# Optimization experiments

Hardware: AMD Instinct MI355X
Metric: run time of the kernel (lower is better)

## Reference

```python
import jax, jax.numpy as jnp
import numpy as np

DELTA_V = 0.5
DELTA_D = 1.5
KSEG = 17  # segment ids 0..16 (0 = background)
EPS = 1e-12


def setup_inputs() -> dict:
    key = jax.random.key(0)
    k1, k2, k3 = jax.random.split(key, 3)
    B, C, H, W = 8, 8, 512, 512
    embeddings = jax.random.normal(k1, (B, C, H, W), dtype=jnp.float32)
    instance_labels = jax.random.randint(k2, (B, H, W), 0, KSEG, dtype=jnp.int32)
    mask = jax.random.randint(k3, (B, H, W), 0, 2, dtype=jnp.int32)
    return {"embeddings": embeddings, "instance_labels": instance_labels, "mask": mask}


def _discriminative_loss(embeddings, inst):
    # embeddings: (B, C, H, W); inst: (B, H, W) int, 0 = ignore/background
    B, C, H, W = embeddings.shape
    N = H * W
    ids = inst.reshape(B, N)
    # global segment ids so one segment_sum handles all batches
    gids = (ids + jnp.arange(B, dtype=ids.dtype)[:, None] * KSEG).reshape(-1)  # (B*N,)
    e = embeddings.reshape(B, C, N).transpose(0, 2, 1).reshape(B * N, C)       # (B*N, C)

    counts = jax.ops.segment_sum(jnp.ones((B * N,), embeddings.dtype), gids, num_segments=B * KSEG)
    sums = jax.ops.segment_sum(e, gids, num_segments=B * KSEG)                 # (B*KSEG, C)
    means = sums / jnp.maximum(counts, 1.0)[:, None]

    # ---- pull: per-pixel hinged distance to its instance mean ----
    diff = e - means[gids]                                                      # (B*N, C)
    d = jnp.sqrt(jnp.maximum(jnp.sum(diff * diff, axis=-1), EPS))               # (B*N,)
    pen = jnp.maximum(d - DELTA_V, 0.0) ** 2
    pen_mean = jax.ops.segment_sum(pen, gids, num_segments=B * KSEG) / jnp.maximum(counts, 1.0)

    counts_bk = counts.reshape(B, KSEG)
    pen_mean_bk = pen_mean.reshape(B, KSEG)
    present = (counts_bk > 0) & (jnp.arange(KSEG)[None, :] != 0)                # (B, KSEG) bool
    presentf = present.astype(embeddings.dtype)
    K = presentf.sum(axis=-1)                                                   # (B,) instances per image
    pull_b = (pen_mean_bk * presentf).sum(axis=-1) / jnp.maximum(K, 1.0)

    # ---- push: hinged pairwise mean distances ----
    mu = means.reshape(B, KSEG, C)
    dm = mu[:, :, None, :] - mu[:, None, :, :]                                  # (B, K, K, C)
    dist = jnp.sqrt(jnp.maximum(jnp.sum(dm * dm, axis=-1), EPS))
    hinge = jnp.maximum(2.0 * DELTA_D - dist, 0.0) ** 2
    iu = jnp.triu(jnp.ones((KSEG, KSEG), bool), k=1)                            # i < j
    pair_mask = (present[:, :, None] & present[:, None, :] & iu[None]).astype(embeddings.dtype)
    n_pairs = pair_mask.sum(axis=(-1, -2))
    push_b = (hinge * pair_mask).sum(axis=(-1, -2)) / jnp.maximum(n_pairs, 1.0)

    validf = (K > 0).astype(embeddings.dtype)
    nvalid = jnp.maximum(validf.sum(), 1.0)
    loss_pull = (pull_b * validf).sum() / nvalid
    loss_push = (push_b * validf).sum() / nvalid
    return loss_pull, loss_push


def reference(embeddings, instance_labels, mask):
    inst = instance_labels * mask  # zero out non-TCL pixels
    return _discriminative_loss(embeddings, inst)
```

## Files before the change

kernel.cpp:

```cpp
#include <hip/hip_runtime.h>

#define BATCH 8
#define CCH 8
#define HW 262144
#define SEGS 16


__global__ __launch_bounds__(256) void accum_kernel(
    const float* __restrict__ emb, const int* __restrict__ lab,
    const int* __restrict__ msk, float* __restrict__ ws)
{
    const int b = blockIdx.y;
    const int wave = threadIdx.x >> 6;
    __shared__ float lsum[4][SEGS][CCH];
    __shared__ float lcnt[4][SEGS];
    for (int i = threadIdx.x; i < 4 * SEGS * CCH; i += 256) (&lsum[0][0][0])[i] = 0.f;
    for (int i = threadIdx.x; i < 4 * SEGS; i += 256) (&lcnt[0][0])[i] = 0.f;
    __syncthreads();

    const float* eb = emb + (size_t)b * CCH * HW;
    const int4* lb = (const int4*)(lab + (size_t)b * HW);
    const int4* mb = (const int4*)(msk + (size_t)b * HW);

    const int ng = HW / 4;
    for (int g = blockIdx.x * 256 + threadIdx.x; g < ng; g += gridDim.x * 256) {
        int4 l4 = lb[g];
        int4 m4 = mb[g];
        int id[4];
        id[0] = m4.x ? l4.x : 0;
        id[1] = m4.y ? l4.y : 0;
        id[2] = m4.z ? l4.z : 0;
        id[3] = m4.w ? l4.w : 0;
#pragma unroll
        for (int j = 0; j < 4; ++j)
            if (id[j]) atomicAdd(&lcnt[wave][id[j] - 1], 1.0f);
#pragma unroll
        for (int c = 0; c < CCH; ++c) {
            float4 e4 = ((const float4*)(eb + (size_t)c * HW))[g];
            float ev[4] = {e4.x, e4.y, e4.z, e4.w};
#pragma unroll
            for (int j = 0; j < 4; ++j)
                if (id[j]) atomicAdd(&lsum[wave][id[j] - 1][c], ev[j]);
        }
    }
    __syncthreads();
    for (int i = threadIdx.x; i < SEGS * CCH; i += 256) {
        float v = (&lsum[0][0][0])[i] + (&lsum[1][0][0])[i]
                + (&lsum[2][0][0])[i] + (&lsum[3][0][0])[i];
        if (v != 0.f) atomicAdd(&ws[128 + b * SEGS * CCH + i], v);
    }
    for (int i = threadIdx.x; i < SEGS; i += 256) {
        float v = lcnt[0][i] + lcnt[1][i] + lcnt[2][i] + lcnt[3][i];
        if (v != 0.f) atomicAdd(&ws[b * SEGS + i], v);
    }
}

__global__ __launch_bounds__(256) void pull_kernel(
    const float* __restrict__ emb, const int* __restrict__ lab,
    const int* __restrict__ msk, float* __restrict__ ws)
{
    const int b = blockIdx.y;
    const int wave = threadIdx.x >> 6;
    __shared__ float mt[CCH][SEGS];
    __shared__ float lpen[4][SEGS];
    for (int i = threadIdx.x; i < 4 * SEGS; i += 256) (&lpen[0][0])[i] = 0.f;
    if (threadIdx.x < SEGS * CCH) {
        int s = threadIdx.x & (SEGS - 1);
        int c = threadIdx.x >> 4;
        float cnt = ws[b * SEGS + s];
        mt[c][s] = ws[128 + (b * SEGS + s) * CCH + c] / fmaxf(cnt, 1.0f);
    }
    __syncthreads();

    const float* eb = emb + (size_t)b * CCH * HW;
    const int4* lb = (const int4*)(lab + (size_t)b * HW);
    const int4* mb = (const int4*)(msk + (size_t)b * HW);

    const int ng = HW / 4;
    for (int g = blockIdx.x * 256 + threadIdx.x; g < ng; g += gridDim.x * 256) {
        int4 l4 = lb[g];
        int4 m4 = mb[g];
        int id[4];
        id[0] = m4.x ? l4.x : 0;
        id[1] = m4.y ? l4.y : 0;
        id[2] = m4.z ? l4.z : 0;
        id[3] = m4.w ? l4.w : 0;
        int ix[4];
#pragma unroll
        for (int j = 0; j < 4; ++j) ix[j] = id[j] ? id[j] - 1 : 0;
        float ss[4] = {0.f, 0.f, 0.f, 0.f};
#pragma unroll
        for (int c = 0; c < CCH; ++c) {
            float4 e4 = ((const float4*)(eb + (size_t)c * HW))[g];
            float ev[4] = {e4.x, e4.y, e4.z, e4.w};
#pragma unroll
            for (int j = 0; j < 4; ++j) {
                float d = ev[j] - mt[c][ix[j]];
                ss[j] += d * d;
            }
        }
#pragma unroll
        for (int j = 0; j < 4; ++j) {
            if (id[j]) {
                float d = sqrtf(fmaxf(ss[j], 1e-12f));
                float h = fmaxf(d - 0.5f, 0.f);
                atomicAdd(&lpen[wave][ix[j]], h * h);
            }
        }
    }
    __syncthreads();
    for (int i = threadIdx.x; i < SEGS; i += 256) {
        float v = lpen[0][i] + lpen[1][i] + lpen[2][i] + lpen[3][i];
        if (v != 0.f) atomicAdd(&ws[1152 + b * SEGS + i], v);
    }
}

__global__ __launch_bounds__(256) void finalize_kernel(
    const float* __restrict__ ws, float* __restrict__ out)
{
    __shared__ float cnt[BATCH][SEGS];
    __shared__ float mu[BATCH][SEGS][CCH];
    __shared__ float pen[BATCH][SEGS];
    __shared__ float res[BATCH][3];

    for (int i = threadIdx.x; i < BATCH * SEGS; i += 256) {
        (&cnt[0][0])[i] = ws[i];
        (&pen[0][0])[i] = ws[1152 + i];
    }
    for (int i = threadIdx.x; i < BATCH * SEGS * CCH; i += 256) {
        float c = ws[i / CCH];
        (&mu[0][0][0])[i] = ws[128 + i] / fmaxf(c, 1.0f);
    }
    __syncthreads();

    const int b = threadIdx.x >> 5;
    const int l = threadIdx.x & 31;

    float pullv = 0.f, Kf = 0.f;
    if (l < SEGS && cnt[b][l] > 0.f) {
        Kf = 1.f;
        pullv = pen[b][l] / cnt[b][l];
    }
    float hs = 0.f, np = 0.f;
    for (int p = l; p < 256; p += 32) {
        int i = p >> 4, j = p & 15;
        if (i < j && cnt[b][i] > 0.f && cnt[b][j] > 0.f) {
            float ssq = 0.f;
#pragma unroll
            for (int c = 0; c < CCH; ++c) {
                float d = mu[b][i][c] - mu[b][j][c];
                ssq += d * d;
            }
            float dist = sqrtf(fmaxf(ssq, 1e-12f));
            float h = fmaxf(3.0f - dist, 0.f);
            hs += h * h;
            np += 1.f;
        }
    }
#pragma unroll
    for (int m = 16; m >= 1; m >>= 1) {
        pullv += __shfl_xor(pullv, m);
        Kf    += __shfl_xor(Kf, m);
        hs    += __shfl_xor(hs, m);
        np    += __shfl_xor(np, m);
    }
    if (l == 0) {
        res[b][0] = (Kf > 0.f) ? pullv / Kf : 0.f;
        res[b][1] = (np > 0.f) ? hs / np : 0.f;
        res[b][2] = (Kf > 0.f) ? 1.f : 0.f;
    }
    __syncthreads();
    if (threadIdx.x == 0) {
        float sp = 0.f, sh = 0.f, nv = 0.f;
        for (int bb = 0; bb < BATCH; ++bb) {
            sp += res[bb][0] * res[bb][2];
            sh += res[bb][1] * res[bb][2];
            nv += res[bb][2];
        }
        nv = fmaxf(nv, 1.f);
        out[0] = sp / nv;
        out[1] = sh / nv;
    }
}

extern "C" void kernel_launch(void* const* d_in, const int* in_sizes, int n_in,
                              void* d_out, int out_size, void* d_ws, size_t ws_size,
                              hipStream_t stream)
{
    const float* emb = (const float*)d_in[0];
    const int* lab = (const int*)d_in[1];
    const int* msk = (const int*)d_in[2];
    float* out = (float*)d_out;
    float* ws = (float*)d_ws;

    hipMemsetAsync(d_ws, 0, 1280 * sizeof(float), stream);
    dim3 grid(128, BATCH);
    accum_kernel<<<grid, 256, 0, stream>>>(emb, lab, msk, ws);
    pull_kernel<<<grid, 256, 0, stream>>>(emb, lab, msk, ws);
    finalize_kernel<<<1, 256, 0, stream>>>(ws, out);
}
```

Measured before the change: 156.7 us.

## Replicate shared histograms per 16 threads and assign one pixel group per thread

Shared-memory histograms for sums, counts and penalties are replicated 16 times per block (one copy per 16 threads) with padded strides, instead of one copy per wave. This is meant to reduce LDS atomic contention when many lanes hit the same segment. The grid doubles so each thread processes exactly one 4-pixel group, removing the grid-stride loop. The cost is a larger final reduction over 16 copies and twice as many global atomics per batch.

Result: slower. 170.8 us (+9.0%).

```diff
diff --git a/kernel.cpp b/kernel.cpp
--- a/kernel.cpp
+++ b/kernel.cpp
@@ -4,6 +4,9 @@
 #define CCH 8
 #define HW 262144
 #define SEGS 16
+#define NREP 16
+#define RSTRIDE 132
+#define CSTRIDE 17
 
 
 __global__ __launch_bounds__(256) void accum_kernel(
@@ -11,47 +14,51 @@
     const int* __restrict__ msk, float* __restrict__ ws)
 {
     const int b = blockIdx.y;
-    const int wave = threadIdx.x >> 6;
-    __shared__ float lsum[4][SEGS][CCH];
-    __shared__ float lcnt[4][SEGS];
-    for (int i = threadIdx.x; i < 4 * SEGS * CCH; i += 256) (&lsum[0][0][0])[i] = 0.f;
-    for (int i = threadIdx.x; i < 4 * SEGS; i += 256) (&lcnt[0][0])[i] = 0.f;
+    const int rep = threadIdx.x >> 4;
+    __shared__ float lsum[NREP * RSTRIDE];
+    __shared__ float lcnt[NREP * CSTRIDE];
+    for (int i = threadIdx.x; i < NREP * RSTRIDE; i += 256) lsum[i] = 0.f;
+    for (int i = threadIdx.x; i < NREP * CSTRIDE; i += 256) lcnt[i] = 0.f;
     __syncthreads();
 
     const float* eb = emb + (size_t)b * CCH * HW;
-    const int4* lb = (const int4*)(lab + (size_t)b * HW);
-    const int4* mb = (const int4*)(msk + (size_t)b * HW);
-
-    const int ng = HW / 4;
-    for (int g = blockIdx.x * 256 + threadIdx.x; g < ng; g += gridDim.x * 256) {
-        int4 l4 = lb[g];
-        int4 m4 = mb[g];
-        int id[4];
-        id[0] = m4.x ? l4.x : 0;
-        id[1] = m4.y ? l4.y : 0;
-        id[2] = m4.z ? l4.z : 0;
-        id[3] = m4.w ? l4.w : 0;
+    const int g = blockIdx.x * 256 + threadIdx.x;
+    int4 l4 = ((const int4*)(lab + (size_t)b * HW))[g];
+    int4 m4 = ((const int4*)(msk + (size_t)b * HW))[g];
+    int id[4];
+    id[0] = m4.x ? l4.x : 0;
+    id[1] = m4.y ? l4.y : 0;
+    id[2] = m4.z ? l4.z : 0;
+    id[3] = m4.w ? l4.w : 0;
+
+    float* ls = lsum + rep * RSTRIDE;
+    float* lc = lcnt + rep * CSTRIDE;
+#pragma unroll
+    for (int j = 0; j < 4; ++j)
+        if (id[j]) atomicAdd(&lc[id[j] - 1], 1.0f);
+#pragma unroll
+    for (int c = 0; c < CCH; ++c) {
+        float4 e4 = ((const float4*)(eb + (size_t)c * HW))[g];
+        float ev[4] = {e4.x, e4.y, e4.z, e4.w};
 #pragma unroll
         for (int j = 0; j < 4; ++j)
-            if (id[j]) atomicAdd(&lcnt[wave][id[j] - 1], 1.0f);
-#pragma unroll
-        for (int c = 0; c < CCH; ++c) {
-            float4 e4 = ((const float4*)(eb + (size_t)c * HW))[g];
-            float ev[4] = {e4.x, e4.y, e4.z, e4.w};
-#pragma unroll
-            for (int j = 0; j < 4; ++j)
-                if (id[j]) atomicAdd(&lsum[wave][id[j] - 1][c], ev[j]);
-        }
-    }
-    __syncthreads();
-    for (int i = threadIdx.x; i < SEGS * CCH; i += 256) {
-        float v = (&lsum[0][0][0])[i] + (&lsum[1][0][0])[i]
-                + (&lsum[2][0][0])[i] + (&lsum[3][0][0])[i];
-        if (v != 0.f) atomicAdd(&ws[128 + b * SEGS * CCH + i], v);
-    }
-    for (int i = threadIdx.x; i < SEGS; i += 256) {
-        float v = lcnt[0][i] + lcnt[1][i] + lcnt[2][i] + lcnt[3][i];
-        if (v != 0.f) atomicAdd(&ws[b * SEGS + i], v);
+            if (id[j]) atomicAdd(&ls[c * SEGS + id[j] - 1], ev[j]);
+    }
+    __syncthreads();
+
+    if (threadIdx.x < SEGS * CCH) {
+        const int i = threadIdx.x;
+        const int c = i >> 4, s = i & 15;
+        float v = 0.f;
+#pragma unroll
+        for (int r = 0; r < NREP; ++r) v += lsum[r * RSTRIDE + i];
+        if (v != 0.f) atomicAdd(&ws[128 + (b * SEGS + s) * CCH + c], v);
+    } else if (threadIdx.x < SEGS * CCH + SEGS) {
+        const int s = threadIdx.x - SEGS * CCH;
+        float v = 0.f;
+#pragma unroll
+        for (int r = 0; r < NREP; ++r) v += lcnt[r * CSTRIDE + s];
+        if (v != 0.f) atomicAdd(&ws[b * SEGS + s], v);
     }
 }
 
@@ -60,10 +67,10 @@
     const int* __restrict__ msk, float* __restrict__ ws)
 {
     const int b = blockIdx.y;
-    const int wave = threadIdx.x >> 6;
+    const int rep = threadIdx.x >> 4;
     __shared__ float mt[CCH][SEGS];
-    __shared__ float lpen[4][SEGS];
-    for (int i = threadIdx.x; i < 4 * SEGS; i += 256) (&lpen[0][0])[i] = 0.f;
+    __shared__ float lpen[NREP * CSTRIDE];
+    for (int i = threadIdx.x; i < NREP * CSTRIDE; i += 256) lpen[i] = 0.f;
     if (threadIdx.x < SEGS * CCH) {
         int s = threadIdx.x & (SEGS - 1);
         int c = threadIdx.x >> 4;
@@ -73,45 +80,45 @@
     __syncthreads();
 
     const float* eb = emb + (size_t)b * CCH * HW;
-    const int4* lb = (const int4*)(lab + (size_t)b * HW);
-    const int4* mb = (const int4*)(msk + (size_t)b * HW);
-
-    const int ng = HW / 4;
-    for (int g = blockIdx.x * 256 + threadIdx.x; g < ng; g += gridDim.x * 256) {
-        int4 l4 = lb[g];
-        int4 m4 = mb[g];
-        int id[4];
-        id[0] = m4.x ? l4.x : 0;
-        id[1] = m4.y ? l4.y : 0;
-        id[2] = m4.z ? l4.z : 0;
-        id[3] = m4.w ? l4.w : 0;
-        int ix[4];
-#pragma unroll
-        for (int j = 0; j < 4; ++j) ix[j] = id[j] ? id[j] - 1 : 0;
-        float ss[4] = {0.f, 0.f, 0.f, 0.f};
-#pragma unroll
-        for (int c = 0; c < CCH; ++c) {
-            float4 e4 = ((const float4*)(eb + (size_t)c * HW))[g];
-            float ev[4] = {e4.x, e4.y, e4.z, e4.w};
-#pragma unroll
-            for (int j = 0; j < 4; ++j) {
-                float d = ev[j] - mt[c][ix[j]];
-                ss[j] += d * d;
-            }
-        }
+    const int g = blockIdx.x * 256 + threadIdx.x;
+    int4 l4 = ((const int4*)(lab + (size_t)b * HW))[g];
+    int4 m4 = ((const int4*)(msk + (size_t)b * HW))[g];
+    int id[4];
+    id[0] = m4.x ? l4.x : 0;
+    id[1] = m4.y ? l4.y : 0;
+    id[2] = m4.z ? l4.z : 0;
+    id[3] = m4.w ? l4.w : 0;
+    int ix[4];
+#pragma unroll
+    for (int j = 0; j < 4; ++j) ix[j] = id[j] ? id[j] - 1 : 0;
+
+    float ss[4] = {0.f, 0.f, 0.f, 0.f};
+#pragma unroll
+    for (int c = 0; c < CCH; ++c) {
+        float4 e4 = ((const float4*)(eb + (size_t)c * HW))[g];
+        float ev[4] = {e4.x, e4.y, e4.z, e4.w};
 #pragma unroll
         for (int j = 0; j < 4; ++j) {
-            if (id[j]) {
-                float d = sqrtf(fmaxf(ss[j], 1e-12f));
-                float h = fmaxf(d - 0.5f, 0.f);
-                atomicAdd(&lpen[wave][ix[j]], h * h);
-            }
-        }
-    }
-    __syncthreads();
-    for (int i = threadIdx.x; i < SEGS; i += 256) {
-        float v = lpen[0][i] + lpen[1][i] + lpen[2][i] + lpen[3][i];
-        if (v != 0.f) atomicAdd(&ws[1152 + b * SEGS + i], v);
+            float d = ev[j] - mt[c][ix[j]];
+            ss[j] += d * d;
+        }
+    }
+    float* lp = lpen + rep * CSTRIDE;
+#pragma unroll
+    for (int j = 0; j < 4; ++j) {
+        if (id[j]) {
+            float d = sqrtf(fmaxf(ss[j], 1e-12f));
+            float h = fmaxf(d - 0.5f, 0.f);
+            atomicAdd(&lp[ix[j]], h * h);
+        }
+    }
+    __syncthreads();
+    if (threadIdx.x < SEGS) {
+        const int s = threadIdx.x;
+        float v = 0.f;
+#pragma unroll
+        for (int r = 0; r < NREP; ++r) v += lpen[r * CSTRIDE + s];
+        if (v != 0.f) atomicAdd(&ws[1152 + b * SEGS + s], v);
     }
 }
 
@@ -194,7 +201,7 @@
     float* ws = (float*)d_ws;
 
     hipMemsetAsync(d_ws, 0, 1280 * sizeof(float), stream);
-    dim3 grid(128, BATCH);
+    dim3 grid(256, BATCH);
     accum_kernel<<<grid, 256, 0, stream>>>(emb, lab, msk, ws);
     pull_kernel<<<grid, 256, 0, stream>>>(emb, lab, msk, ws);
     finalize_kernel<<<1, 256, 0, stream>>>(ws, out);
```

## Unroll grid-stride loops into two prefetched iterations and pad shared arrays

Applied to the files above, without the earlier changes.

Both the accumulate and pull kernels replace their grid-stride loops with a fixed two-iteration body whose label, mask and embedding loads are all issued up front, so more memory requests are in flight per thread. Shared accumulators are padded (stride 9 / 17) to reduce bank conflicts. In the pull kernel, the mean table is replicated into four copies indexed by 16-lane group to spread LDS bank contention. The kernels now hard-assume HW/4 == 2*GX*256 and raise register pressure by holding 16 float4 embedding values per thread.

Result: no change. 159.2 us (+1.6%).

```diff
diff --git a/kernel.cpp b/kernel.cpp
--- a/kernel.cpp
+++ b/kernel.cpp
@@ -4,6 +4,7 @@
 #define CCH 8
 #define HW 262144
 #define SEGS 16
+#define GX 128
 
 
 __global__ __launch_bounds__(256) void accum_kernel(
@@ -12,46 +13,60 @@
 {
     const int b = blockIdx.y;
     const int wave = threadIdx.x >> 6;
-    __shared__ float lsum[4][SEGS][CCH];
-    __shared__ float lcnt[4][SEGS];
-    for (int i = threadIdx.x; i < 4 * SEGS * CCH; i += 256) (&lsum[0][0][0])[i] = 0.f;
-    for (int i = threadIdx.x; i < 4 * SEGS; i += 256) (&lcnt[0][0])[i] = 0.f;
-    __syncthreads();
-
-    const float* eb = emb + (size_t)b * CCH * HW;
+    __shared__ float lsum[4][SEGS][9];
+    __shared__ float lcnt[4][SEGS + 1];
+    for (int i = threadIdx.x; i < 4 * SEGS * 9; i += 256) (&lsum[0][0][0])[i] = 0.f;
+    for (int i = threadIdx.x; i < 4 * (SEGS + 1); i += 256) (&lcnt[0][0])[i] = 0.f;
+    __syncthreads();
+
+    const float* ebase = emb + (size_t)b * CCH * HW;
     const int4* lb = (const int4*)(lab + (size_t)b * HW);
     const int4* mb = (const int4*)(msk + (size_t)b * HW);
 
-    const int ng = HW / 4;
-    for (int g = blockIdx.x * 256 + threadIdx.x; g < ng; g += gridDim.x * 256) {
-        int4 l4 = lb[g];
-        int4 m4 = mb[g];
-        int id[4];
-        id[0] = m4.x ? l4.x : 0;
-        id[1] = m4.y ? l4.y : 0;
-        id[2] = m4.z ? l4.z : 0;
-        id[3] = m4.w ? l4.w : 0;
-#pragma unroll
-        for (int j = 0; j < 4; ++j)
-            if (id[j]) atomicAdd(&lcnt[wave][id[j] - 1], 1.0f);
-#pragma unroll
-        for (int c = 0; c < CCH; ++c) {
-            float4 e4 = ((const float4*)(eb + (size_t)c * HW))[g];
-            float ev[4] = {e4.x, e4.y, e4.z, e4.w};
-#pragma unroll
-            for (int j = 0; j < 4; ++j)
-                if (id[j]) atomicAdd(&lsum[wave][id[j] - 1][c], ev[j]);
-        }
-    }
-    __syncthreads();
-    for (int i = threadIdx.x; i < SEGS * CCH; i += 256) {
-        float v = (&lsum[0][0][0])[i] + (&lsum[1][0][0])[i]
-                + (&lsum[2][0][0])[i] + (&lsum[3][0][0])[i];
-        if (v != 0.f) atomicAdd(&ws[128 + b * SEGS * CCH + i], v);
-    }
-    for (int i = threadIdx.x; i < SEGS; i += 256) {
-        float v = lcnt[0][i] + lcnt[1][i] + lcnt[2][i] + lcnt[3][i];
-        if (v != 0.f) atomicAdd(&ws[b * SEGS + i], v);
+    const int g0 = blockIdx.x * 256 + threadIdx.x;
+    const int g1 = g0 + GX * 256;
+
+    int4 l40 = lb[g0], l41 = lb[g1];
+    int4 m40 = mb[g0], m41 = mb[g1];
+    float4 e0[CCH], e1[CCH];
+#pragma unroll
+    for (int c = 0; c < CCH; ++c) {
+        const float4* p = (const float4*)(ebase + (size_t)c * HW);
+        e0[c] = p[g0];
+        e1[c] = p[g1];
+    }
+
+    int id0[4], id1[4];
+    id0[0] = m40.x ? l40.x : 0;  id0[1] = m40.y ? l40.y : 0;
+    id0[2] = m40.z ? l40.z : 0;  id0[3] = m40.w ? l40.w : 0;
+    id1[0] = m41.x ? l41.x : 0;  id1[1] = m41.y ? l41.y : 0;
+    id1[2] = m41.z ? l41.z : 0;  id1[3] = m41.w ? l41.w : 0;
+
+    float* ls = &lsum[wave][0][0];
+    float* lc = &lcnt[wave][0];
+#pragma unroll
+    for (int j = 0; j < 4; ++j) {
+        if (id0[j]) atomicAdd(&lc[id0[j] - 1], 1.0f);
+        if (id1[j]) atomicAdd(&lc[id1[j] - 1], 1.0f);
+    }
+#pragma unroll
+    for (int c = 0; c < CCH; ++c) {
+#pragma unroll
+        for (int j = 0; j < 4; ++j) {
+            if (id0[j]) atomicAdd(&ls[(id0[j] - 1) * 9 + c], ((const float*)&e0[c])[j]);
+            if (id1[j]) atomicAdd(&ls[(id1[j] - 1) * 9 + c], ((const float*)&e1[c])[j]);
+        }
+    }
+    __syncthreads();
+
+    if (threadIdx.x < SEGS * CCH) {
+        const int s = threadIdx.x >> 3, c = threadIdx.x & 7;
+        float v = lsum[0][s][c] + lsum[1][s][c] + lsum[2][s][c] + lsum[3][s][c];
+        if (v != 0.f) atomicAdd(&ws[128 + (b * SEGS + s) * CCH + c], v);
+    } else if (threadIdx.x < SEGS * CCH + SEGS) {
+        const int s = threadIdx.x - SEGS * CCH;
+        float v = lcnt[0][s] + lcnt[1][s] + lcnt[2][s] + lcnt[3][s];
+        if (v != 0.f) atomicAdd(&ws[b * SEGS + s], v);
     }
 }
 
@@ -60,58 +75,79 @@
     const int* __restrict__ msk, float* __restrict__ ws)
 {
     const int b = blockIdx.y;
-    const int wave = threadIdx.x >> 6;
-    __shared__ float mt[CCH][SEGS];
-    __shared__ float lpen[4][SEGS];
-    for (int i = threadIdx.x; i < 4 * SEGS; i += 256) (&lpen[0][0])[i] = 0.f;
+    const int grp = (threadIdx.x >> 4) & 3;
+    __shared__ float mtr[4][CCH][SEGS + 1];
+    __shared__ float lpen[4][SEGS + 1];
+    for (int i = threadIdx.x; i < 4 * (SEGS + 1); i += 256) (&lpen[0][0])[i] = 0.f;
     if (threadIdx.x < SEGS * CCH) {
-        int s = threadIdx.x & (SEGS - 1);
-        int c = threadIdx.x >> 4;
+        const int s = threadIdx.x & 15, c = threadIdx.x >> 4;
         float cnt = ws[b * SEGS + s];
-        mt[c][s] = ws[128 + (b * SEGS + s) * CCH + c] / fmaxf(cnt, 1.0f);
-    }
-    __syncthreads();
-
-    const float* eb = emb + (size_t)b * CCH * HW;
+        float m = ws[128 + (b * SEGS + s) * CCH + c] / fmaxf(cnt, 1.0f);
+        mtr[0][c][s] = m; mtr[1][c][s] = m; mtr[2][c][s] = m; mtr[3][c][s] = m;
+    }
+    __syncthreads();
+
+    const float* ebase = emb + (size_t)b * CCH * HW;
     const int4* lb = (const int4*)(lab + (size_t)b * HW);
     const int4* mb = (const int4*)(msk + (size_t)b * HW);
 
-    const int ng = HW / 4;
-    for (int g = blockIdx.x * 256 + threadIdx.x; g < ng; g += gridDim.x * 256) {
-        int4 l4 = lb[g];
-        int4 m4 = mb[g];
-        int id[4];
-        id[0] = m4.x ? l4.x : 0;
-        id[1] = m4.y ? l4.y : 0;
-        id[2] = m4.z ? l4.z : 0;
-        id[3] = m4.w ? l4.w : 0;
-        int ix[4];
-#pragma unroll
-        for (int j = 0; j < 4; ++j) ix[j] = id[j] ? id[j] - 1 : 0;
-        float ss[4] = {0.f, 0.f, 0.f, 0.f};
-#pragma unroll
-        for (int c = 0; c < CCH; ++c) {
-            float4 e4 = ((const float4*)(eb + (size_t)c * HW))[g];
-            float ev[4] = {e4.x, e4.y, e4.z, e4.w};
-#pragma unroll
-            for (int j = 0; j < 4; ++j) {
-                float d = ev[j] - mt[c][ix[j]];
-                ss[j] += d * d;
-            }
-        }
+    const int g0 = blockIdx.x * 256 + threadIdx.x;
+    const int g1 = g0 + GX * 256;
+
+    int4 l40 = lb[g0], l41 = lb[g1];
+    int4 m40 = mb[g0], m41 = mb[g1];
+    float4 e0[CCH], e1[CCH];
+#pragma unroll
+    for (int c = 0; c < CCH; ++c) {
+        const float4* p = (const float4*)(ebase + (size_t)c * HW);
+        e0[c] = p[g0];
+        e1[c] = p[g1];
+    }
+
+    int id0[4], id1[4];
+    id0[0] = m40.x ? l40.x : 0;  id0[1] = m40.y ? l40.y : 0;
+    id0[2] = m40.z ? l40.z : 0;  id0[3] = m40.w ? l40.w : 0;
+    id1[0] = m41.x ? l41.x : 0;  id1[1] = m41.y ? l41.y : 0;
+    id1[2] = m41.z ? l41.z : 0;  id1[3] = m41.w ? l41.w : 0;
+    int ix0[4], ix1[4];
+#pragma unroll
+    for (int j = 0; j < 4; ++j) {
+        ix0[j] = id0[j] ? id0[j] - 1 : 0;
+        ix1[j] = id1[j] ? id1[j] - 1 : 0;
+    }
+
+    const float (*mt)[SEGS + 1] = mtr[grp];
+    float ss0[4] = {0.f, 0.f, 0.f, 0.f};
+    float ss1[4] = {0.f, 0.f, 0.f, 0.f};
+#pragma unroll
+    for (int c = 0; c < CCH; ++c) {
 #pragma unroll
         for (int j = 0; j < 4; ++j) {
-            if (id[j]) {
-                float d = sqrtf(fmaxf(ss[j], 1e-12f));
-                float h = fmaxf(d - 0.5f, 0.f);
-                atomicAdd(&lpen[wave][ix[j]], h * h);
-            }
-        }
-    }
-    __syncthreads();
-    for (int i = threadIdx.x; i < SEGS; i += 256) {
-        float v = lpen[0][i] + lpen[1][i] + lpen[2][i] + lpen[3][i];
-        if (v != 0.f) atomicAdd(&ws[1152 + b * SEGS + i], v);
+            float d0 = ((const float*)&e0[c])[j] - mt[c][ix0[j]];
+            ss0[j] += d0 * d0;
+            float d1 = ((const float*)&e1[c])[j] - mt[c][ix1[j]];
+            ss1[j] += d1 * d1;
+        }
+    }
+    float* lp = &lpen[grp][0];
+#pragma unroll
+    for (int j = 0; j < 4; ++j) {
+        if (id0[j]) {
+            float d = sqrtf(fmaxf(ss0[j], 1e-12f));
+            float h = fmaxf(d - 0.5f, 0.f);
+            atomicAdd(&lp[ix0[j]], h * h);
+        }
+        if (id1[j]) {
+            float d = sqrtf(fmaxf(ss1[j], 1e-12f));
+            float h = fmaxf(d - 0.5f, 0.f);
+            atomicAdd(&lp[ix1[j]], h * h);
+        }
+    }
+    __syncthreads();
+    if (threadIdx.x < SEGS) {
+        const int s = threadIdx.x;
+        float v = lpen[0][s] + lpen[1][s] + lpen[2][s] + lpen[3][s];
+        if (v != 0.f) atomicAdd(&ws[1152 + b * SEGS + s], v);
     }
 }
 
@@ -194,7 +230,7 @@
     float* ws = (float*)d_ws;
 
     hipMemsetAsync(d_ws, 0, 1280 * sizeof(float), stream);
-    dim3 grid(128, BATCH);
+    dim3 grid(GX, BATCH);
     accum_kernel<<<grid, 256, 0, stream>>>(emb, lab, msk, ws);
     pull_kernel<<<grid, 256, 0, stream>>>(emb, lab, msk, ws);
     finalize_kernel<<<1, 256, 0, stream>>>(ws, out);
```

## Replace LDS atomics with register one-hot accumulation and wave shuffle reductions

Applied to the files above, without the earlier changes.

The accumulate and pull kernels no longer use shared-memory atomic histograms. Each thread now keeps per-segment sums in registers, adding into every segment through a one-hot mask, and the partial sums are combined with xor-shuffle wave reductions before a few global atomics. In the accumulate kernel each wave handles two channels, and the pull kernel keeps all 128 segment means in registers, picking the right one with a select tree instead of an LDS gather. The grid is halved and each block covers a fixed span, which trades many more ALU ops and high register pressure for removing atomic contention.

After: 327.7 us. 2.09x slower.

```diff
diff --git a/kernel.cpp b/kernel.cpp
--- a/kernel.cpp
+++ b/kernel.cpp
@@ -4,114 +4,163 @@
 #define CCH 8
 #define HW 262144
 #define SEGS 16
-
-
-__global__ __launch_bounds__(256) void accum_kernel(
+#define BX 64
+
+__device__ __forceinline__ void fadd(float* p, float v) { unsafeAtomicAdd(p, v); }
+
+
+__global__ __launch_bounds__(256, 4) void accum_kernel(
     const float* __restrict__ emb, const int* __restrict__ lab,
     const int* __restrict__ msk, float* __restrict__ ws)
 {
     const int b = blockIdx.y;
-    const int wave = threadIdx.x >> 6;
-    __shared__ float lsum[4][SEGS][CCH];
-    __shared__ float lcnt[4][SEGS];
-    for (int i = threadIdx.x; i < 4 * SEGS * CCH; i += 256) (&lsum[0][0][0])[i] = 0.f;
-    for (int i = threadIdx.x; i < 4 * SEGS; i += 256) (&lcnt[0][0])[i] = 0.f;
-    __syncthreads();
-
-    const float* eb = emb + (size_t)b * CCH * HW;
+    const int w = threadIdx.x >> 6;
+    const int lane = threadIdx.x & 63;
+    const int c0 = 2 * w;
+
+    const float4* e0p = (const float4*)(emb + ((size_t)b * CCH + c0) * HW);
+    const float4* e1p = (const float4*)(emb + ((size_t)b * CCH + c0 + 1) * HW);
     const int4* lb = (const int4*)(lab + (size_t)b * HW);
     const int4* mb = (const int4*)(msk + (size_t)b * HW);
 
-    const int ng = HW / 4;
-    for (int g = blockIdx.x * 256 + threadIdx.x; g < ng; g += gridDim.x * 256) {
-        int4 l4 = lb[g];
-        int4 m4 = mb[g];
-        int id[4];
-        id[0] = m4.x ? l4.x : 0;
-        id[1] = m4.y ? l4.y : 0;
-        id[2] = m4.z ? l4.z : 0;
-        id[3] = m4.w ? l4.w : 0;
-#pragma unroll
-        for (int j = 0; j < 4; ++j)
-            if (id[j]) atomicAdd(&lcnt[wave][id[j] - 1], 1.0f);
-#pragma unroll
-        for (int c = 0; c < CCH; ++c) {
-            float4 e4 = ((const float4*)(eb + (size_t)c * HW))[g];
-            float ev[4] = {e4.x, e4.y, e4.z, e4.w};
-#pragma unroll
-            for (int j = 0; j < 4; ++j)
-                if (id[j]) atomicAdd(&lsum[wave][id[j] - 1][c], ev[j]);
-        }
-    }
-    __syncthreads();
-    for (int i = threadIdx.x; i < SEGS * CCH; i += 256) {
-        float v = (&lsum[0][0][0])[i] + (&lsum[1][0][0])[i]
-                + (&lsum[2][0][0])[i] + (&lsum[3][0][0])[i];
-        if (v != 0.f) atomicAdd(&ws[128 + b * SEGS * CCH + i], v);
-    }
-    for (int i = threadIdx.x; i < SEGS; i += 256) {
-        float v = lcnt[0][i] + lcnt[1][i] + lcnt[2][i] + lcnt[3][i];
-        if (v != 0.f) atomicAdd(&ws[b * SEGS + i], v);
-    }
-}
-
-__global__ __launch_bounds__(256) void pull_kernel(
+    float acc0[SEGS], acc1[SEGS];
+    float cnt[4];
+#pragma unroll
+    for (int s = 0; s < SEGS; ++s) { acc0[s] = 0.f; acc1[s] = 0.f; }
+    cnt[0] = cnt[1] = cnt[2] = cnt[3] = 0.f;
+    const int csbase = 4 * w + 1;
+
+    const int qbase = blockIdx.x * 1024;
+#pragma unroll 2
+    for (int it = 0; it < 16; ++it) {
+        const int q = qbase + it * 64 + lane;
+        int4 l4 = lb[q];
+        int4 m4 = mb[q];
+        float4 e04 = e0p[q];
+        float4 e14 = e1p[q];
+        int id[4] = { m4.x ? l4.x : 0, m4.y ? l4.y : 0, m4.z ? l4.z : 0, m4.w ? l4.w : 0 };
+        float ev0[4] = {e04.x, e04.y, e04.z, e04.w};
+        float ev1[4] = {e14.x, e14.y, e14.z, e14.w};
+#pragma unroll
+        for (int j = 0; j < 4; ++j) {
+            const int idj = id[j];
+            const float a = ev0[j], bb = ev1[j];
+#pragma unroll
+            for (int s = 0; s < SEGS; ++s) {
+                float m = (idj == s + 1) ? 1.f : 0.f;
+                acc0[s] += m * a;
+                acc1[s] += m * bb;
+            }
+#pragma unroll
+            for (int k = 0; k < 4; ++k)
+                cnt[k] += (idj == csbase + k) ? 1.f : 0.f;
+        }
+    }
+
+#pragma unroll
+    for (int m = 1; m < 64; m <<= 1) {
+#pragma unroll
+        for (int s = 0; s < SEGS; ++s) {
+            acc0[s] += __shfl_xor(acc0[s], m);
+            acc1[s] += __shfl_xor(acc1[s], m);
+        }
+#pragma unroll
+        for (int k = 0; k < 4; ++k) cnt[k] += __shfl_xor(cnt[k], m);
+    }
+
+    if (lane == 0) {
+        float* sums = ws + 128 + (size_t)b * SEGS * CCH;
+#pragma unroll
+        for (int s = 0; s < SEGS; ++s) {
+            if (acc0[s] != 0.f) fadd(&sums[s * CCH + c0], acc0[s]);
+            if (acc1[s] != 0.f) fadd(&sums[s * CCH + c0 + 1], acc1[s]);
+        }
+#pragma unroll
+        for (int k = 0; k < 4; ++k)
+            if (cnt[k] != 0.f) fadd(&ws[b * SEGS + 4 * w + k], cnt[k]);
+    }
+}
+
+__global__ __launch_bounds__(256, 2) void pull_kernel(
     const float* __restrict__ emb, const int* __restrict__ lab,
     const int* __restrict__ msk, float* __restrict__ ws)
 {
     const int b = blockIdx.y;
-    const int wave = threadIdx.x >> 6;
-    __shared__ float mt[CCH][SEGS];
-    __shared__ float lpen[4][SEGS];
-    for (int i = threadIdx.x; i < 4 * SEGS; i += 256) (&lpen[0][0])[i] = 0.f;
-    if (threadIdx.x < SEGS * CCH) {
-        int s = threadIdx.x & (SEGS - 1);
-        int c = threadIdx.x >> 4;
-        float cnt = ws[b * SEGS + s];
-        mt[c][s] = ws[128 + (b * SEGS + s) * CCH + c] / fmaxf(cnt, 1.0f);
-    }
-    __syncthreads();
-
-    const float* eb = emb + (size_t)b * CCH * HW;
+    const int lane = threadIdx.x & 63;
+
+    float mu[SEGS][CCH];
+#pragma unroll
+    for (int s = 0; s < SEGS; ++s) {
+        float cv = ws[b * SEGS + s];
+        float inv = 1.0f / fmaxf(cv, 1.0f);
+#pragma unroll
+        for (int c = 0; c < CCH; ++c)
+            mu[s][c] = ws[128 + (b * SEGS + s) * CCH + c] * inv;
+    }
+
+    float pen[SEGS];
+#pragma unroll
+    for (int s = 0; s < SEGS; ++s) pen[s] = 0.f;
+
+    const float* ebase = emb + (size_t)b * CCH * HW;
     const int4* lb = (const int4*)(lab + (size_t)b * HW);
     const int4* mb = (const int4*)(msk + (size_t)b * HW);
 
-    const int ng = HW / 4;
-    for (int g = blockIdx.x * 256 + threadIdx.x; g < ng; g += gridDim.x * 256) {
-        int4 l4 = lb[g];
-        int4 m4 = mb[g];
-        int id[4];
-        id[0] = m4.x ? l4.x : 0;
-        id[1] = m4.y ? l4.y : 0;
-        id[2] = m4.z ? l4.z : 0;
-        id[3] = m4.w ? l4.w : 0;
-        int ix[4];
-#pragma unroll
-        for (int j = 0; j < 4; ++j) ix[j] = id[j] ? id[j] - 1 : 0;
-        float ss[4] = {0.f, 0.f, 0.f, 0.f};
-#pragma unroll
-        for (int c = 0; c < CCH; ++c) {
-            float4 e4 = ((const float4*)(eb + (size_t)c * HW))[g];
-            float ev[4] = {e4.x, e4.y, e4.z, e4.w};
-#pragma unroll
-            for (int j = 0; j < 4; ++j) {
-                float d = ev[j] - mt[c][ix[j]];
-                ss[j] += d * d;
+#pragma unroll
+    for (int k = 0; k < 4; ++k) {
+        const int q = blockIdx.x * 1024 + k * 256 + threadIdx.x;
+        int4 l4 = lb[q];
+        int4 m4 = mb[q];
+        float4 e4[CCH];
+#pragma unroll
+        for (int c = 0; c < CCH; ++c)
+            e4[c] = ((const float4*)(ebase + (size_t)c * HW))[q];
+        int id[4] = { m4.x ? l4.x : 0, m4.y ? l4.y : 0, m4.z ? l4.z : 0, m4.w ? l4.w : 0 };
+#pragma unroll
+        for (int j = 0; j < 4; ++j) {
+            const int idj = id[j];
+            const int ix = (idj > 0) ? idj - 1 : 0;
+            const bool b0 = ix & 1, b1 = ix & 2, b2 = ix & 4, b3 = ix & 8;
+            float ss = 0.f;
+#pragma unroll
+            for (int c = 0; c < CCH; ++c) {
+                float s01 = b0 ? mu[1][c]  : mu[0][c];
+                float s23 = b0 ? mu[3][c]  : mu[2][c];
+                float s45 = b0 ? mu[5][c]  : mu[4][c];
+                float s67 = b0 ? mu[7][c]  : mu[6][c];
+                float s89 = b0 ? mu[9][c]  : mu[8][c];
+                float sab = b0 ? mu[11][c] : mu[10][c];
+                float scd = b0 ? mu[13][c] : mu[12][c];
+                float sef = b0 ? mu[15][c] : mu[14][c];
+                float t0 = b1 ? s23 : s01;
+                float t1 = b1 ? s67 : s45;
+                float t2 = b1 ? sab : s89;
+                float t3 = b1 ? sef : scd;
+                float u0 = b2 ? t1 : t0;
+                float u1 = b2 ? t3 : t2;
+                float mv = b3 ? u1 : u0;
+                float d = ((const float*)&e4[c])[j] - mv;
+                ss += d * d;
             }
-        }
-#pragma unroll
-        for (int j = 0; j < 4; ++j) {
-            if (id[j]) {
-                float d = sqrtf(fmaxf(ss[j], 1e-12f));
-                float h = fmaxf(d - 0.5f, 0.f);
-                atomicAdd(&lpen[wave][ix[j]], h * h);
-            }
-        }
-    }
-    __syncthreads();
-    for (int i = threadIdx.x; i < SEGS; i += 256) {
-        float v = lpen[0][i] + lpen[1][i] + lpen[2][i] + lpen[3][i];
-        if (v != 0.f) atomicAdd(&ws[1152 + b * SEGS + i], v);
+            float d = sqrtf(fmaxf(ss, 1e-12f));
+            float h = fmaxf(d - 0.5f, 0.f);
+            float h2 = h * h;
+#pragma unroll
+            for (int s = 0; s < SEGS; ++s)
+                pen[s] += (idj == s + 1) ? h2 : 0.f;
+        }
+    }
+
+#pragma unroll
+    for (int m = 1; m < 64; m <<= 1)
+#pragma unroll
+        for (int s = 0; s < SEGS; ++s)
+            pen[s] += __shfl_xor(pen[s], m);
+
+    if (lane == 0) {
+#pragma unroll
+        for (int s = 0; s < SEGS; ++s)
+            if (pen[s] != 0.f) fadd(&ws[1152 + b * SEGS + s], pen[s]);
     }
 }
 
@@ -194,7 +243,7 @@
     float* ws = (float*)d_ws;
 
     hipMemsetAsync(d_ws, 0, 1280 * sizeof(float), stream);
-    dim3 grid(128, BATCH);
+    dim3 grid(BX, BATCH);
     accum_kernel<<<grid, 256, 0, stream>>>(emb, lab, msk, ws);
     pull_kernel<<<grid, 256, 0, stream>>>(emb, lab, msk, ws);
     finalize_kernel<<<1, 256, 0, stream>>>(ws, out);
```
